# Kernel tuning notes

Measured on AMD Instinct MI355X. Metric: run time of the kernel, lower is better.

## Reference

```python
import jax, jax.numpy as jnp
import numpy as np

B, LQ, LK, D = 4, 2048, 2048, 512
EPS = 1e-8  # torch cosine_similarity eps


def setup_inputs() -> dict:
    key = jax.random.key(0)
    ks = jax.random.split(key, 8)
    s = 1.0 / np.sqrt(D)
    return {
        "query": jax.random.normal(ks[0], (B, LQ, D), jnp.float32),
        "key": jax.random.normal(ks[1], (B, LK, D), jnp.float32),
        "value": jax.random.normal(ks[2], (B, LK, D), jnp.float32),
        "Wq": jax.random.normal(ks[3], (D, D), jnp.float32) * s,
        "bq": jax.random.normal(ks[4], (D,), jnp.float32) * s,
        "Wk": jax.random.normal(ks[5], (D, D), jnp.float32) * s,
        "bk": jax.random.normal(ks[6], (D,), jnp.float32) * s,
        "scoring_weights": jnp.ones((3,), jnp.float32) / 3.0,
    }


def reference(query, key, value, Wq, bq, Wk, bk, scoring_weights):
    # fused tanh-QK transforms (torch Linear: x @ W.T + b)
    q = jnp.tanh(jnp.einsum('bqd,ed->bqe', query, Wq) + bq)  # [B,LQ,D]
    k = jnp.tanh(jnp.einsum('bkd,ed->bke', key, Wk) + bk)    # [B,LK,D]

    dot = jnp.einsum('bqd,bkd->bqk', q, k)                   # [B,LQ,LK]
    qn = jnp.linalg.norm(q, axis=-1)                         # [B,LQ]
    kn = jnp.linalg.norm(k, axis=-1)                         # [B,LK]
    # cosine_similarity: dot / max(|q|*|k|, eps)
    cos = dot / jnp.maximum(qn[:, :, None] * kn[:, None, :], EPS)
    # -cdist (p=2): sqrt(|q|^2 + |k|^2 - 2 q.k), clamped at 0
    sq = jnp.maximum(qn[:, :, None] ** 2 + kn[:, None, :] ** 2 - 2.0 * dot, 0.0)
    euc = -jnp.sqrt(sq)

    w = jax.nn.softmax(scoring_weights)
    scores = w[0] * dot + w[1] * cos + w[2] * euc
    attn = jax.nn.softmax(scores, axis=-1)                   # [B,LQ,LK]
    context = jnp.einsum('bqk,bkd->bqd', attn, value)        # [B,LQ,D]
    return context, attn
```

## Files before the change

kernel.cpp:

```cpp
#include <hip/hip_runtime.h>
#include <cstdint>
#include <cstddef>

namespace {

constexpr int BATCH = 4;
constexpr int LQ = 2048;
constexpr int LK = 2048;
constexpr int D = 512;
constexpr int MQ = BATCH * LQ;

using f16 = _Float16;
typedef _Float16 f16x8 __attribute__((ext_vector_type(8)));
typedef _Float16 f16x4 __attribute__((ext_vector_type(4)));
typedef float f32x4 __attribute__((ext_vector_type(4)));

__device__ __forceinline__ f16x8 cvt8(const float4 a, const float4 b) {
  f16x8 h;
  h[0] = (f16)a.x; h[1] = (f16)a.y; h[2] = (f16)a.z; h[3] = (f16)a.w;
  h[4] = (f16)b.x; h[5] = (f16)b.y; h[6] = (f16)b.z; h[7] = (f16)b.w;
  return h;
}

typedef __attribute__((address_space(1))) const void gas_void;
typedef __attribute__((address_space(3))) void las_void;
__device__ __forceinline__ void gload_lds16(const void* g, void* l) {
  __builtin_amdgcn_global_load_lds((gas_void*)g, (las_void*)l, 16, 0, 0);
}

__global__ __launch_bounds__(256) void prep_kernel(
    const float* __restrict__ query, const float* __restrict__ keyp,
    const float* __restrict__ value, const float* __restrict__ Wq,
    const float* __restrict__ Wk, const float* __restrict__ bq,
    const float* __restrict__ bk, f16* __restrict__ qh, f16* __restrict__ kh,
    float* __restrict__ qnsqp, float* __restrict__ knsqp,
    f16* __restrict__ vt) {
  __shared__ __align__(16) char smem[21504];
  const int bid0 = blockIdx.x;
  const int t = threadIdx.x;

  if (bid0 >= 512) {
    const int bid = bid0 - 512;
    const int kt = bid & 31;
    const int dt = (bid >> 5) & 7;
    const int b = bid >> 8;
    const int k0 = kt * 64, d0 = dt * 64;
    f16(*T)[72] = reinterpret_cast<f16(*)[72]>(smem);
#pragma unroll
    for (int i = 0; i < 4; ++i) {
      const int u = t + i * 256;
      const int k = u >> 4;
      const int d4 = (u & 15) << 2;
      float4 x = *reinterpret_cast<const float4*>(
          value + (size_t)(b * LK + k0 + k) * D + d0 + d4);
      T[d4 + 0][k] = (f16)x.x;
      T[d4 + 1][k] = (f16)x.y;
      T[d4 + 2][k] = (f16)x.z;
      T[d4 + 3][k] = (f16)x.w;
    }
    __syncthreads();
#pragma unroll
    for (int i = 0; i < 2; ++i) {
      const int u = t + i * 256;
      const int d = u >> 3;
      const int k8 = (u & 7) << 3;
      f16x8 h = *reinterpret_cast<const f16x8*>(&T[d][k8]);
      *reinterpret_cast<f16x8*>(vt + (size_t)(b * D + d0 + d) * LK + k0 + k8) =
          h;
    }
    return;
  }

  const int which = bid0 >> 8;
  const float* __restrict__ X = which ? keyp : query;
  const float* __restrict__ W = which ? Wk : Wq;
  const float* __restrict__ bias = which ? bk : bq;
  f16* __restrict__ out = which ? kh : qh;
  float* __restrict__ nsqp = which ? knsqp : qnsqp;

  const int bid = bid0 & 255;
  const int tm = bid & 63;
  const int tn = bid >> 6;
  const int brow = tm * 128, bcol = tn * 128;
  const int lane = t & 63;
  const int wid = t >> 6;
  const int wr = (wid >> 1) * 64, wc = (wid & 1) * 64;
  const int lr = lane & 15;
  const int lk = (lane >> 4) << 3;
  const int g4 = (lane >> 4) << 2;

  f16(*As)[40] = reinterpret_cast<f16(*)[40]>(smem);
  f16(*Bs)[40] = reinterpret_cast<f16(*)[40]>(smem + 10240);
  float(*s_ss)[2] = reinterpret_cast<float(*)[2]>(smem + 20480);

  f32x4 acc[4][4] = {};

  for (int k0 = 0; k0 < D; k0 += 32) {
#pragma unroll
    for (int i = 0; i < 2; ++i) {
      const int u = t + i * 256;
      const int r = u >> 2;
      const int c8 = (u & 3) << 3;
      const float4* pa =
          reinterpret_cast<const float4*>(X + (size_t)(brow + r) * D + k0 + c8);
      *reinterpret_cast<f16x8*>(&As[r][c8]) = cvt8(pa[0], pa[1]);
      const float4* pb =
          reinterpret_cast<const float4*>(W + (size_t)(bcol + r) * D + k0 + c8);
      *reinterpret_cast<f16x8*>(&Bs[r][c8]) = cvt8(pb[0], pb[1]);
    }
    __syncthreads();
    f16x8 af[4], bf[4];
#pragma unroll
    for (int m = 0; m < 4; ++m)
      af[m] = *reinterpret_cast<const f16x8*>(&As[wr + m * 16 + lr][lk]);
#pragma unroll
    for (int n = 0; n < 4; ++n)
      bf[n] = *reinterpret_cast<const f16x8*>(&Bs[wc + n * 16 + lr][lk]);
#pragma unroll
    for (int m = 0; m < 4; ++m)
#pragma unroll
      for (int n = 0; n < 4; ++n)
        acc[m][n] =
            __builtin_amdgcn_mfma_f32_16x16x32_f16(bf[n], af[m], acc[m][n], 0, 0, 0);
    __syncthreads();
  }

  float4 bv[4];
#pragma unroll
  for (int n = 0; n < 4; ++n)
    bv[n] = *reinterpret_cast<const float4*>(&bias[bcol + wc + n * 16 + g4]);

#pragma unroll
  for (int m = 0; m < 4; ++m) {
    const int row = brow + wr + m * 16 + lr;
    float ss = 0.f;
#pragma unroll
    for (int n = 0; n < 4; ++n) {
      float th[4];
#pragma unroll
      for (int r = 0; r < 4; ++r) {
        th[r] = tanhf(acc[m][n][r] + ((const float*)&bv[n])[r]);
        ss = fmaf(th[r], th[r], ss);
      }
      f16x4 h4;
      h4[0] = (f16)th[0]; h4[1] = (f16)th[1];
      h4[2] = (f16)th[2]; h4[3] = (f16)th[3];
      *reinterpret_cast<f16x4*>(out + (size_t)row * D + bcol + wc + n * 16 + g4) =
          h4;
    }
    ss += __shfl_xor(ss, 16);
    ss += __shfl_xor(ss, 32);
    if (lane < 16) s_ss[wr + m * 16 + lr][wid & 1] = ss;
  }
  __syncthreads();
  if (t < 128) nsqp[(size_t)(brow + t) * 4 + tn] = s_ss[t][0] + s_ss[t][1];
}

template <bool RAW16>
__global__ __launch_bounds__(256, 2) void scores_kernel(
    const f16* __restrict__ qh, const f16* __restrict__ kh,
    const float* __restrict__ qnsqp, const float* __restrict__ knsqp,
    const float* __restrict__ sw, float* __restrict__ attn,
    f16* __restrict__ sraw, float2* __restrict__ tstats) {
  const int bid0 = blockIdx.x;
  const int bid = (bid0 & 7) * 128 + (bid0 >> 3);
  const int tn = bid & 15;
  const int tm = (bid >> 4) & 15;
  const int b = bid >> 8;
  const int brow = tm * 128, bcol = tn * 128;
  const int t = threadIdx.x;
  const int lane = t & 63;
  const int wid = t >> 6;
  const int wr = (wid >> 1) * 64, wc = (wid & 1) * 64;
  const int lr = lane & 15;
  const int lk = (lane >> 4) << 3;
  const int g4 = (lane >> 4) << 2;

  __shared__ f16 As[128 * 64];
  __shared__ f16 Bs[128 * 64];
  __shared__ float s_m[128][2];
  __shared__ float s_l[128][2];

  f32x4 acc[4][4] = {};

  const int srow = lane >> 3;
  const int scol = ((lane & 7) ^ srow) << 4;
  const char* aBase = (const char*)(qh + (size_t)(b * LQ + brow) * D);
  const char* bBase = (const char*)(kh + (size_t)(b * LK + bcol) * D);
  const int swz = (lr & 7) << 4;

  for (int k0 = 0; k0 < D; k0 += 64) {
#pragma unroll
    for (int i = 0; i < 4; ++i) {
      const int chunk = wid * 4 + i;
      const int row = chunk * 8 + srow;
      gload_lds16(aBase + (size_t)row * (D * 2) + k0 * 2 + scol,
                  (char*)As + chunk * 1024);
      gload_lds16(bBase + (size_t)row * (D * 2) + k0 * 2 + scol,
                  (char*)Bs + chunk * 1024);
    }
    __syncthreads();
    f16x8 af[2][4], bf[2][4];
#pragma unroll
    for (int h = 0; h < 2; ++h) {
      const int cb = h * 64 + lk * 2;
#pragma unroll
      for (int m = 0; m < 4; ++m)
        af[h][m] = *(const f16x8*)((const char*)As + (wr + m * 16 + lr) * 128 +
                                   (cb ^ swz));
#pragma unroll
      for (int n = 0; n < 4; ++n)
        bf[h][n] = *(const f16x8*)((const char*)Bs + (wc + n * 16 + lr) * 128 +
                                   (cb ^ swz));
    }
#pragma unroll
    for (int h = 0; h < 2; ++h)
#pragma unroll
      for (int m = 0; m < 4; ++m)
#pragma unroll
        for (int n = 0; n < 4; ++n)
          acc[m][n] = __builtin_amdgcn_mfma_f32_16x16x32_f16(bf[h][n], af[h][m],
                                                             acc[m][n], 0, 0, 0);
    __syncthreads();
  }

  const float s0 = sw[0], s1 = sw[1], s2 = sw[2];
  const float smx = fmaxf(s0, fmaxf(s1, s2));
  float w0 = __expf(s0 - smx), w1 = __expf(s1 - smx), w2 = __expf(s2 - smx);
  const float winv = 1.f / (w0 + w1 + w2);
  w0 *= winv; w1 *= winv; w2 *= winv;

  float qn2_[4], w1rq[4];
#pragma unroll
  for (int m = 0; m < 4; ++m) {
    const float4 qp = *reinterpret_cast<const float4*>(
        &qnsqp[(size_t)(b * LQ + brow + wr + m * 16 + lr) * 4]);
    const float v = (qp.x + qp.y) + (qp.z + qp.w);
    qn2_[m] = v;
    w1rq[m] = w1 * rsqrtf(fmaxf(v, 1e-16f));
  }
  float kn2[4][4], rk[4][4];
#pragma unroll
  for (int n = 0; n < 4; ++n) {
#pragma unroll
    for (int r = 0; r < 4; ++r) {
      const int col = bcol + wc + n * 16 + g4 + r;
      const float4 kp = *reinterpret_cast<const float4*>(
          &knsqp[(size_t)(b * LK + col) * 4]);
      const float v = (kp.x + kp.y) + (kp.z + kp.w);
      kn2[n][r] = v;
      rk[n][r] = rsqrtf(fmaxf(v, 1e-16f));
    }
  }

#pragma unroll
  for (int m = 0; m < 4; ++m) {
    const int row = brow + wr + m * 16 + lr;
    float mx = -3.4e38f;
#pragma unroll
    for (int n = 0; n < 4; ++n) {
      float4 o;
#pragma unroll
      for (int r = 0; r < 4; ++r) {
        const float dot = acc[m][n][r];
        const float qk2 = qn2_[m] + kn2[n][r];
        const float st = sqrtf(fmaxf(qk2 - 2.f * dot, 0.f));
        const float c = fmaf(w1rq[m], rk[n][r], w0);
        const float s = fmaf(dot, c, -w2 * st);
        ((float*)&o)[r] = s;
        acc[m][n][r] = s;
        mx = fmaxf(mx, s);
      }
      if constexpr (RAW16) {
        f16x4 h4;
        h4[0] = (f16)o.x; h4[1] = (f16)o.y; h4[2] = (f16)o.z; h4[3] = (f16)o.w;
        *reinterpret_cast<f16x4*>(sraw + (size_t)(b * LQ + row) * LK + bcol +
                                  wc + n * 16 + g4) = h4;
      } else {
        *reinterpret_cast<float4*>(attn + (size_t)(b * LQ + row) * LK + bcol +
                                   wc + n * 16 + g4) = o;
      }
    }
    mx = fmaxf(mx, __shfl_xor(mx, 16));
    mx = fmaxf(mx, __shfl_xor(mx, 32));
    float es = 0.f;
#pragma unroll
    for (int n = 0; n < 4; ++n)
#pragma unroll
      for (int r = 0; r < 4; ++r) es += __expf(acc[m][n][r] - mx);
    es += __shfl_xor(es, 16);
    es += __shfl_xor(es, 32);
    if (lane < 16) {
      s_m[wr + m * 16 + lr][wid & 1] = mx;
      s_l[wr + m * 16 + lr][wid & 1] = es;
    }
  }
  __syncthreads();
  if (t < 128) {
    const float m0 = s_m[t][0], m1 = s_m[t][1];
    const float M = fmaxf(m0, m1);
    const float L = s_l[t][0] * __expf(m0 - M) + s_l[t][1] * __expf(m1 - M);
    tstats[(size_t)(b * LQ + brow + t) * 16 + tn] = make_float2(M, L);
  }
}

__global__ __launch_bounds__(256) void normalize_kernel(
    float* __restrict__ attn, const float2* __restrict__ tstats) {
  const int row = blockIdx.x;
  const int t = threadIdx.x;
  __shared__ float sM, sI;
  if (t < 16) {
    float2 st = tstats[(size_t)row * 16 + t];
    float M = st.x;
    M = fmaxf(M, __shfl_xor(M, 8));
    M = fmaxf(M, __shfl_xor(M, 4));
    M = fmaxf(M, __shfl_xor(M, 2));
    M = fmaxf(M, __shfl_xor(M, 1));
    float l = st.y * __expf(st.x - M);
    l += __shfl_xor(l, 8);
    l += __shfl_xor(l, 4);
    l += __shfl_xor(l, 2);
    l += __shfl_xor(l, 1);
    if (t == 0) { sM = M; sI = 1.f / l; }
  }
  __syncthreads();
  const float M = sM, invL = sI;
  float* rp = attn + (size_t)row * LK + t * 8;
  float4 v0 = *reinterpret_cast<const float4*>(rp);
  float4 v1 = *reinterpret_cast<const float4*>(rp + 4);
  v0.x = __expf(v0.x - M) * invL; v0.y = __expf(v0.y - M) * invL;
  v0.z = __expf(v0.z - M) * invL; v0.w = __expf(v0.w - M) * invL;
  v1.x = __expf(v1.x - M) * invL; v1.y = __expf(v1.y - M) * invL;
  v1.z = __expf(v1.z - M) * invL; v1.w = __expf(v1.w - M) * invL;
  *reinterpret_cast<float4*>(rp) = v0;
  *reinterpret_cast<float4*>(rp + 4) = v1;
}

template <bool NORM>
__global__ __launch_bounds__(256, 2) void pv_kernel(
    float* __restrict__ attnf, const f16* __restrict__ sraw,
    const f16* __restrict__ vt, const float2* __restrict__ tstats,
    float* __restrict__ ctx) {
  const int bid0 = blockIdx.x;
  const int bid = (bid0 & 7) * 128 + (bid0 >> 3);
  const int tn = bid & 3;
  const int tm = (bid >> 2) & 63;
  const int b = bid >> 8;
  const int brow = tm * 32, bcol = tn * 128;
  const int t = threadIdx.x;
  const int lane = t & 63;
  const int wid = t >> 6;
  const int wr = (wid >> 1) * 16, wc = (wid & 1) * 64;
  const int lr = lane & 15;
  const int lk = (lane >> 4) << 3;
  const int g4 = (lane >> 4) << 2;

  __shared__ f16 As[32 * 64];
  __shared__ f16 Bs[128 * 64];
  __shared__ float sMl[32], sIl[32];

  f32x4 acc[4] = {};

  const int srow = lane >> 3;
  const int scol = ((lane & 7) ^ srow) << 4;
  const size_t arow0 = (size_t)(b * LQ + brow);
  const char* bBase = (const char*)(vt + (size_t)(b * D + bcol) * LK);
  const int swz = (lr & 7) << 4;

  const int arow = t >> 3;
  const int c16 = (t & 7) << 4;
  const int csrc = c16 ^ ((arow & 7) << 4);
  const char* aRow =
      (const char*)sraw + (arow0 + arow) * (size_t)LK * 2 + csrc;
  float Mr = 0.f, Ir = 0.f;

  if constexpr (NORM) {
    if (t < 128) {
      const int prow = t >> 2;
      const int j4 = (t & 3) * 4;
      const float4* tp =
          reinterpret_cast<const float4*>(&tstats[(arow0 + prow) * 16 + j4]);
      const float4 a = tp[0], c = tp[1];
      float m_ = fmaxf(fmaxf(a.x, a.z), fmaxf(c.x, c.z));
      m_ = fmaxf(m_, __shfl_xor(m_, 1));
      m_ = fmaxf(m_, __shfl_xor(m_, 2));
      float l_ = a.y * __expf(a.x - m_) + a.w * __expf(a.z - m_) +
                 c.y * __expf(c.x - m_) + c.w * __expf(c.z - m_);
      l_ += __shfl_xor(l_, 1);
      l_ += __shfl_xor(l_, 2);
      if ((t & 3) == 0) {
        sMl[prow] = m_;
        sIl[prow] = 1.f / l_;
      }
    }
    __syncthreads();
    Mr = sMl[arow];
    Ir = sIl[arow];
  }

  f16x8 hcur;
  if constexpr (NORM) hcur = *(const f16x8*)(aRow);

  for (int k0 = 0; k0 < LK; k0 += 64) {
#pragma unroll
    for (int i = 0; i < 4; ++i) {
      const int chunk = wid * 4 + i;
      const int row = chunk * 8 + srow;
      gload_lds16(bBase + (size_t)row * (LK * 2) + k0 * 2 + scol,
                  (char*)Bs + chunk * 1024);
    }
    if constexpr (NORM) {
      f16x8 hnext;
      if (k0 + 64 < LK) hnext = *(const f16x8*)(aRow + (k0 + 64) * 2);
      float4 e0, e1;
      e0.x = __expf((float)hcur[0] - Mr) * Ir;
      e0.y = __expf((float)hcur[1] - Mr) * Ir;
      e0.z = __expf((float)hcur[2] - Mr) * Ir;
      e0.w = __expf((float)hcur[3] - Mr) * Ir;
      e1.x = __expf((float)hcur[4] - Mr) * Ir;
      e1.y = __expf((float)hcur[5] - Mr) * Ir;
      e1.z = __expf((float)hcur[6] - Mr) * Ir;
      e1.w = __expf((float)hcur[7] - Mr) * Ir;
      *(f16x8*)((char*)As + arow * 128 + c16) = cvt8(e0, e1);
      if ((k0 >> 9) == tn) {
        float* op = attnf + (arow0 + arow) * LK + k0 + (csrc >> 1);
        *reinterpret_cast<float4*>(op) = e0;
        *reinterpret_cast<float4*>(op + 4) = e1;
      }
      hcur = hnext;
    } else {
      const int u = t;
      const int row = u >> 3;
      const float4* ps = (const float4*)((const char*)attnf +
                                         ((arow0 + row) * LK + k0) * 4 +
                                         csrc * 2);
      *(f16x8*)((char*)As + row * 128 + c16) = cvt8(ps[0], ps[1]);
    }
    __syncthreads();
    f16x8 af[2], bf[2][4];
#pragma unroll
    for (int h = 0; h < 2; ++h) {
      const int cb = h * 64 + lk * 2;
      af[h] = *(const f16x8*)((const char*)As + (wr + lr) * 128 + (cb ^ swz));
#pragma unroll
      for (int n = 0; n < 4; ++n)
        bf[h][n] = *(const f16x8*)((const char*)Bs + (wc + n * 16 + lr) * 128 +
                                   (cb ^ swz));
    }
#pragma unroll
    for (int h = 0; h < 2; ++h)
#pragma unroll
      for (int n = 0; n < 4; ++n)
        acc[n] = __builtin_amdgcn_mfma_f32_16x16x32_f16(bf[h][n], af[h],
                                                        acc[n], 0, 0, 0);
    __syncthreads();
  }

  const int row = brow + wr + lr;
  float* rowp = ctx + (size_t)(b * LQ + row) * D + bcol + wc;
#pragma unroll
  for (int n = 0; n < 4; ++n) {
    float4 o;
    o.x = acc[n][0]; o.y = acc[n][1];
    o.z = acc[n][2]; o.w = acc[n][3];
    *reinterpret_cast<float4*>(rowp + n * 16 + g4) = o;
  }
}

}

extern "C" void kernel_launch(void* const* d_in, const int* in_sizes, int n_in,
                              void* d_out, int out_size, void* d_ws,
                              size_t ws_size, hipStream_t stream) {
  const float* query = (const float*)d_in[0];
  const float* key = (const float*)d_in[1];
  const float* value = (const float*)d_in[2];
  const float* Wq = (const float*)d_in[3];
  const float* bq = (const float*)d_in[4];
  const float* Wk = (const float*)d_in[5];
  const float* bk = (const float*)d_in[6];
  const float* sw = (const float*)d_in[7];

  float* ctx = (float*)d_out;
  float* attn = (float*)d_out + (size_t)BATCH * LQ * D;

  char* ws = (char*)d_ws;
  f16* vt = (f16*)ws;
  f16* qh = (f16*)(ws + (size_t)(8u << 20));
  f16* kh = (f16*)(ws + (size_t)(16u << 20));
  float* qnsqp = (float*)(ws + (size_t)(24u << 20));
  float* knsqp = qnsqp + (size_t)MQ * 4;
  float2* tstats = (float2*)(ws + (size_t)(25u << 20));
  f16* sraw = (f16*)(ws + (size_t)(26u << 20));
  const size_t ws_needed =
      ((size_t)(26u << 20)) + (size_t)BATCH * LQ * LK * sizeof(f16);
  const bool useA16 = ws_size >= ws_needed;

  prep_kernel<<<1536, 256, 0, stream>>>(query, key, value, Wq, Wk, bq, bk, qh,
                                        kh, qnsqp, knsqp, vt);
  if (useA16) {
    scores_kernel<true><<<1024, 256, 0, stream>>>(qh, kh, qnsqp, knsqp, sw,
                                                  attn, sraw, tstats);
    pv_kernel<true><<<1024, 256, 0, stream>>>(attn, sraw, vt, tstats, ctx);
  } else {
    scores_kernel<false><<<1024, 256, 0, stream>>>(qh, kh, qnsqp, knsqp, sw,
                                                   attn, sraw, tstats);
    normalize_kernel<<<MQ, 256, 0, stream>>>(attn, tstats);
    pv_kernel<false><<<1024, 256, 0, stream>>>(attn, sraw, vt, tstats, ctx);
  }
}
```

Before: 108.4 us.

## Store tile-local exp in fp16 and rescale per tile in PV kernel

The scores kernel now reduces the tile max across both warps first, then writes exp(s - tile_max) as fp16 instead of raw scores. It emits the tile max and plain sum as stats. The PV kernel precomputes one scale factor exp(M_tile - M_row)/L per row and tile, so the inner loop does a single fp16 vector multiply instead of eight expf calls. Occupancy hints for both kernels go from 2 to 4 blocks per SM, which may force register spills. Rounding the exp values and the scale to fp16 before the product also adds some precision error.

```diff
diff --git a/kernel.cpp b/kernel.cpp
--- a/kernel.cpp
+++ b/kernel.cpp
@@ -157,7 +157,7 @@
 }
 
 template <bool RAW16>
-__global__ __launch_bounds__(256, 2) void scores_kernel(
+__global__ __launch_bounds__(256, 4) void scores_kernel(
     const f16* __restrict__ qh, const f16* __restrict__ kh,
     const float* __restrict__ qnsqp, const float* __restrict__ knsqp,
     const float* __restrict__ sw, float* __restrict__ attn,
@@ -255,7 +255,8 @@
 
 #pragma unroll
   for (int m = 0; m < 4; ++m) {
-    const int row = brow + wr + m * 16 + lr;
+    const int rl = wr + m * 16 + lr;
+    const int row = brow + rl;
     float mx = -3.4e38f;
 #pragma unroll
     for (int n = 0; n < 4; ++n) {
@@ -271,36 +272,45 @@
         acc[m][n][r] = s;
         mx = fmaxf(mx, s);
       }
-      if constexpr (RAW16) {
-        f16x4 h4;
-        h4[0] = (f16)o.x; h4[1] = (f16)o.y; h4[2] = (f16)o.z; h4[3] = (f16)o.w;
-        *reinterpret_cast<f16x4*>(sraw + (size_t)(b * LQ + row) * LK + bcol +
-                                  wc + n * 16 + g4) = h4;
-      } else {
+      if constexpr (!RAW16) {
         *reinterpret_cast<float4*>(attn + (size_t)(b * LQ + row) * LK + bcol +
                                    wc + n * 16 + g4) = o;
       }
     }
     mx = fmaxf(mx, __shfl_xor(mx, 16));
     mx = fmaxf(mx, __shfl_xor(mx, 32));
+    if (lane < 16) s_m[rl][wid & 1] = mx;
+  }
+  __syncthreads();
+
+#pragma unroll
+  for (int m = 0; m < 4; ++m) {
+    const int rl = wr + m * 16 + lr;
+    const int row = brow + rl;
+    const float Mt = fmaxf(s_m[rl][0], s_m[rl][1]);
     float es = 0.f;
 #pragma unroll
-    for (int n = 0; n < 4; ++n)
-#pragma unroll
-      for (int r = 0; r < 4; ++r) es += __expf(acc[m][n][r] - mx);
+    for (int n = 0; n < 4; ++n) {
+      float e0 = __expf(acc[m][n][0] - Mt);
+      float e1 = __expf(acc[m][n][1] - Mt);
+      float e2 = __expf(acc[m][n][2] - Mt);
+      float e3 = __expf(acc[m][n][3] - Mt);
+      es += (e0 + e1) + (e2 + e3);
+      if constexpr (RAW16) {
+        f16x4 h4;
+        h4[0] = (f16)e0; h4[1] = (f16)e1; h4[2] = (f16)e2; h4[3] = (f16)e3;
+        *reinterpret_cast<f16x4*>(sraw + (size_t)(b * LQ + row) * LK + bcol +
+                                  wc + n * 16 + g4) = h4;
+      }
+    }
     es += __shfl_xor(es, 16);
     es += __shfl_xor(es, 32);
-    if (lane < 16) {
-      s_m[wr + m * 16 + lr][wid & 1] = mx;
-      s_l[wr + m * 16 + lr][wid & 1] = es;
-    }
+    if (lane < 16) s_l[rl][wid & 1] = es;
   }
   __syncthreads();
   if (t < 128) {
-    const float m0 = s_m[t][0], m1 = s_m[t][1];
-    const float M = fmaxf(m0, m1);
-    const float L = s_l[t][0] * __expf(m0 - M) + s_l[t][1] * __expf(m1 - M);
-    tstats[(size_t)(b * LQ + brow + t) * 16 + tn] = make_float2(M, L);
+    tstats[(size_t)(b * LQ + brow + t) * 16 + tn] =
+        make_float2(fmaxf(s_m[t][0], s_m[t][1]), s_l[t][0] + s_l[t][1]);
   }
 }
 
@@ -337,7 +347,7 @@
 }
 
 template <bool NORM>
-__global__ __launch_bounds__(256, 2) void pv_kernel(
+__global__ __launch_bounds__(256, 4) void pv_kernel(
     float* __restrict__ attnf, const f16* __restrict__ sraw,
     const f16* __restrict__ vt, const float2* __restrict__ tstats,
     float* __restrict__ ctx) {
@@ -357,7 +367,7 @@
 
   __shared__ f16 As[32 * 64];
   __shared__ f16 Bs[128 * 64];
-  __shared__ float sMl[32], sIl[32];
+  __shared__ float sScale[32][17];
 
   f32x4 acc[4] = {};
 
@@ -372,7 +382,6 @@
   const int csrc = c16 ^ ((arow & 7) << 4);
   const char* aRow =
       (const char*)sraw + (arow0 + arow) * (size_t)LK * 2 + csrc;
-  float Mr = 0.f, Ir = 0.f;
 
   if constexpr (NORM) {
     if (t < 128) {
@@ -388,14 +397,13 @@
                  c.y * __expf(c.x - m_) + c.w * __expf(c.z - m_);
       l_ += __shfl_xor(l_, 1);
       l_ += __shfl_xor(l_, 2);
-      if ((t & 3) == 0) {
-        sMl[prow] = m_;
-        sIl[prow] = 1.f / l_;
-      }
-    }
-    __syncthreads();
-    Mr = sMl[arow];
-    Ir = sIl[arow];
+      const float invL = 1.f / l_;
+      sScale[prow][j4 + 0] = __expf(a.x - m_) * invL;
+      sScale[prow][j4 + 1] = __expf(a.z - m_) * invL;
+      sScale[prow][j4 + 2] = __expf(c.x - m_) * invL;
+      sScale[prow][j4 + 3] = __expf(c.z - m_) * invL;
+    }
+    __syncthreads();
   }
 
   f16x8 hcur;
@@ -412,29 +420,27 @@
     if constexpr (NORM) {
       f16x8 hnext;
       if (k0 + 64 < LK) hnext = *(const f16x8*)(aRow + (k0 + 64) * 2);
-      float4 e0, e1;
-      e0.x = __expf((float)hcur[0] - Mr) * Ir;
-      e0.y = __expf((float)hcur[1] - Mr) * Ir;
-      e0.z = __expf((float)hcur[2] - Mr) * Ir;
-      e0.w = __expf((float)hcur[3] - Mr) * Ir;
-      e1.x = __expf((float)hcur[4] - Mr) * Ir;
-      e1.y = __expf((float)hcur[5] - Mr) * Ir;
-      e1.z = __expf((float)hcur[6] - Mr) * Ir;
-      e1.w = __expf((float)hcur[7] - Mr) * Ir;
-      *(f16x8*)((char*)As + arow * 128 + c16) = cvt8(e0, e1);
+      const float sc = sScale[arow][k0 >> 7];
+      const f16 sch = (f16)sc;
+      const f16x8 scv = {sch, sch, sch, sch, sch, sch, sch, sch};
+      const f16x8 hv = hcur * scv;
+      *(f16x8*)((char*)As + arow * 128 + c16) = hv;
       if ((k0 >> 9) == tn) {
+        float4 e0, e1;
+        e0.x = (float)hv[0]; e0.y = (float)hv[1];
+        e0.z = (float)hv[2]; e0.w = (float)hv[3];
+        e1.x = (float)hv[4]; e1.y = (float)hv[5];
+        e1.z = (float)hv[6]; e1.w = (float)hv[7];
         float* op = attnf + (arow0 + arow) * LK + k0 + (csrc >> 1);
         *reinterpret_cast<float4*>(op) = e0;
         *reinterpret_cast<float4*>(op + 4) = e1;
       }
       hcur = hnext;
     } else {
-      const int u = t;
-      const int row = u >> 3;
       const float4* ps = (const float4*)((const char*)attnf +
-                                         ((arow0 + row) * LK + k0) * 4 +
+                                         ((arow0 + arow) * LK + k0) * 4 +
                                          csrc * 2);
-      *(f16x8*)((char*)As + row * 128 + c16) = cvt8(ps[0], ps[1]);
+      *(f16x8*)((char*)As + arow * 128 + c16) = cvt8(ps[0], ps[1]);
     }
     __syncthreads();
     f16x8 af[2], bf[2][4];
```

Result: faster. 106.0 us (-2.2%).
